# Kernel tuning notes

Hardware: AMD Instinct MI355X
Metric: run time of the kernel (lower is better)

## Reference

```python
import jax, jax.numpy as jnp
import numpy as np

B, N, I = 2, 2048, 768   # batch, note_seq_len, input_size
C, D = 256, 64           # num_classes, max_desc_len
LN_EPS = 1e-5


def setup_inputs() -> dict:
    key = jax.random.key(0)
    ks = jax.random.split(key, 10)
    x = jax.random.normal(ks[0], (B, N, I), dtype=jnp.float32)
    attention_masks = jnp.ones((B, N), dtype=jnp.int32)
    desc_emb = jax.random.normal(ks[1], (C, D, I), dtype=jnp.float32)
    # description mask: first token always valid, rest random 0/1
    dm_rest = jax.random.randint(ks[2], (C, D - 1), 0, 2, dtype=jnp.int32)
    desc_mask = jnp.concatenate([jnp.ones((C, 1), dtype=jnp.int32), dm_rest], axis=1)
    std = 0.03
    Wq = std * jax.random.normal(ks[3], (I, I), dtype=jnp.float32)
    Wk = std * jax.random.normal(ks[4], (I, I), dtype=jnp.float32)
    Wv = std * jax.random.normal(ks[5], (I, I), dtype=jnp.float32)
    Wo = std * jax.random.normal(ks[6], (1, I), dtype=jnp.float32)
    bo = jnp.zeros((1,), dtype=jnp.float32)
    ln_g = jnp.ones((I,), dtype=jnp.float32)
    ln_b = jnp.zeros((I,), dtype=jnp.float32)
    return {"x": x, "attention_masks": attention_masks, "desc_emb": desc_emb,
            "desc_mask": desc_mask, "Wq": Wq, "Wk": Wk, "Wv": Wv,
            "Wo": Wo, "bo": bo, "ln_g": ln_g, "ln_b": ln_b}


def reference(x, attention_masks, desc_emb, desc_mask, Wq, Wk, Wv, Wo, bo, ln_g, ln_b):
    scale = 1.0 / np.sqrt(np.float32(I))
    # projections (nn.Linear: y = x @ W.T)
    q = jnp.einsum('cdi,ji->cdj', desc_emb, Wq)        # [C, D, I]
    k = jnp.einsum('bni,ji->bnj', x, Wk)               # [B, N, I]
    v = jnp.einsum('bni,ji->bnj', x, Wv)               # [B, N, I]
    # cross-attention scores: [B, C, D, N]
    scores = jnp.einsum('cdi,bni->bcdn', q, k) * scale
    # double mask: desc token validity x note token validity
    mask = (desc_mask[None, :, :, None] * attention_masks[:, None, None, :]) > 0
    scores = jnp.where(mask, scores, jnp.float32(-1e9))
    attn = jax.nn.softmax(scores, axis=-1)             # over note tokens
    ctx = jnp.einsum('bcdn,bni->bcdi', attn, v)        # [B, C, D, I]
    dmask_f = (desc_mask > 0).astype(ctx.dtype)        # [C, D]
    ctx = ctx * dmask_f[None, :, :, None]
    denom = dmask_f.sum(axis=1)[None, :, None]          # [1, C, 1]
    pooled = ctx.sum(axis=2) / denom                    # [B, C, I]
    # layernorm over feature dim
    mu = pooled.mean(axis=-1, keepdims=True)
    var = jnp.mean((pooled - mu) ** 2, axis=-1, keepdims=True)
    y = (pooled - mu) * jax.lax.rsqrt(var + LN_EPS) * ln_g + ln_b
    out = jnp.einsum('bci,i->bc', y, Wo[0]) + bo[0]     # [B, C]
    return out
```

## Files before the change

### kernel.cpp

```cpp
#include <hip/hip_runtime.h>
#include <hip/hip_bf16.h>

#define BB 2
#define NN 2048
#define II 768
#define CC 256
#define DD 64
#define MM (CC * DD)

typedef __attribute__((ext_vector_type(8))) short short8;
typedef __attribute__((ext_vector_type(4))) float f32x4;

static constexpr float SCALE = 0.036084391824351615f;

__device__ __forceinline__ unsigned short f2bf(float f) {
  union { float f; unsigned int u; } v; v.f = f;
  unsigned int u = v.u;
  unsigned int r = u + 0x7fffu + ((u >> 16) & 1u);
  return (unsigned short)(r >> 16);
}
__device__ __forceinline__ float bf2f(unsigned short h) {
  union { unsigned int u; float f; } v; v.u = ((unsigned int)h) << 16;
  return v.f;
}

union U8 { unsigned short us[8]; uint4 v; };
struct US4 { unsigned short x, y, z, w; };

#define GLOAD_LDS16(gp, lp)                                                    \
  __builtin_amdgcn_global_load_lds(                                            \
      (const __attribute__((address_space(1))) unsigned int*)(gp),             \
      (__attribute__((address_space(3))) unsigned int*)(lp), 16, 0, 0)

__global__ __launch_bounds__(256)
void cvt_scan_kernel(const float* __restrict__ demb, const float* __restrict__ x,
                     const float* __restrict__ Wq, const float* __restrict__ Wk,
                     const float* __restrict__ Wv, const int* __restrict__ dmask,
                     unsigned short* __restrict__ Qb, unsigned short* __restrict__ xb,
                     unsigned short* __restrict__ Wqb, unsigned short* __restrict__ Wkb,
                     unsigned short* __restrict__ Wvb,
                     int* __restrict__ idx, int* __restrict__ cstart,
                     int* __restrict__ ccnt, int* __restrict__ meta)
{
  if (blockIdx.x == gridDim.x - 1) {
    const int c = threadIdx.x;
    int4 dmv[16];
    const int4* src = (const int4*)(dmask + c * 64);
    int cnt = 0;
    #pragma unroll
    for (int u = 0; u < 16; ++u) {
      dmv[u] = src[u];
      cnt += (dmv[u].x != 0) + (dmv[u].y != 0) + (dmv[u].z != 0) + (dmv[u].w != 0);
    }
    __shared__ int s[256];
    s[c] = cnt;
    __syncthreads();
    for (int off = 1; off < 256; off <<= 1) {
      int v = (c >= off) ? s[c - off] : 0;
      __syncthreads();
      s[c] += v;
      __syncthreads();
    }
    const int excl = s[c] - cnt;
    cstart[c] = excl;
    ccnt[c] = cnt;
    int j = excl;
    #pragma unroll
    for (int u = 0; u < 16; ++u) {
      if (dmv[u].x) idx[j++] = c * 64 + u * 4 + 0;
      if (dmv[u].y) idx[j++] = c * 64 + u * 4 + 1;
      if (dmv[u].z) idx[j++] = c * 64 + u * 4 + 2;
      if (dmv[u].w) idx[j++] = c * 64 + u * 4 + 3;
    }
    if (c == 255) {
      int mv = s[255];
      int mpad = (mv + 127) & ~127;
      for (int t = mv; t < mpad; ++t) idx[t] = 0;
      meta[0] = mpad;
    }
  }
  const int NF_DEMB = 3145728;
  const int NF_X    = 786432;
  const int NF_W    = 147456;
  const int NF_TOT  = NF_DEMB + NF_X + 3 * NF_W;
  for (int i = blockIdx.x * 256 + threadIdx.x; i < NF_TOT; i += gridDim.x * 256) {
    const float* src; unsigned short* dst; int off;
    if (i < NF_DEMB) {
      if (dmask[i / 192] == 0) continue;
      src = demb; dst = Qb; off = i;
    }
    else if (i < NF_DEMB + NF_X) { src = x; dst = xb; off = i - NF_DEMB; }
    else if (i < NF_DEMB + NF_X + NF_W) { src = Wq; dst = Wqb; off = i - NF_DEMB - NF_X; }
    else if (i < NF_DEMB + NF_X + 2 * NF_W) { src = Wk; dst = Wkb; off = i - NF_DEMB - NF_X - NF_W; }
    else { src = Wv; dst = Wvb; off = i - NF_DEMB - NF_X - 2 * NF_W; }
    float4 v = *(const float4*)(src + (size_t)off * 4);
    US4 o; o.x = f2bf(v.x); o.y = f2bf(v.y); o.z = f2bf(v.z); o.w = f2bf(v.w);
    *(US4*)(dst + (size_t)off * 4) = o;
  }
}

__global__ __launch_bounds__(256, 2)
void proj3(const unsigned short* __restrict__ Qb,
           const unsigned short* __restrict__ xb,
           const unsigned short* __restrict__ Wqb,
           const unsigned short* __restrict__ Wkb,
           const unsigned short* __restrict__ Wvb,
           unsigned short* __restrict__ Qp,
           unsigned short* __restrict__ Kp,
           unsigned short* __restrict__ Vt,
           const int* __restrict__ gidx, const int* __restrict__ meta)
{
  const int T = blockIdx.x;
  const int j0 = (T % 6) * 128;
  const int t = T / 6;
  const int mode = (t < 128) ? 0 : ((t < 160) ? 1 : 2);
  const int m0 = (mode == 0 ? t : (mode == 1 ? t - 128 : t - 160)) * 128;
  if (mode == 0 && m0 >= meta[0]) return;
  const unsigned short* A = (mode == 0) ? Qb : xb;
  const unsigned short* W = (mode == 0) ? Wqb : (mode == 1 ? Wkb : Wvb);

  const int tid = threadIdx.x;
  const int lane = tid & 63, wv = tid >> 6;
  const int lrow = lane & 15, khi = lane >> 4;
  const int wr = wv >> 1, wc = wv & 1;

  __shared__ __align__(16) unsigned short smem[128 * 128];
  unsigned short* a_lds = smem;
  unsigned short* b_lds = smem + 128 * 64;

  int rowsrc[4];
  #pragma unroll
  for (int u = 0; u < 4; ++u) {
    int row = m0 + ((u * 256 + tid) >> 3);
    rowsrc[u] = (mode == 0) ? gidx[row] : row;
  }

  f32x4 acc[4][4] = {};

  for (int kc = 0; kc < 12; ++kc) {
    const int k0 = kc * 64;
    __syncthreads();
    #pragma unroll
    for (int u = 0; u < 4; ++u) {
      int idx = u * 256 + tid;
      int row = idx >> 3, g = idx & 7;
      int sg = g ^ (row & 7);
      GLOAD_LDS16(A + (size_t)rowsrc[u] * II + k0 + sg * 8, &a_lds[idx * 8]);
      GLOAD_LDS16(W + (size_t)(j0 + row) * II + k0 + sg * 8, &b_lds[idx * 8]);
    }
    __syncthreads();
    #pragma unroll
    for (int s = 0; s < 2; ++s) {
      short8 af[4], bf[4];
      #pragma unroll
      for (int m = 0; m < 4; ++m) {
        int ar = wr * 64 + m * 16 + lrow;
        int g = s * 4 + khi;
        af[m] = *(const short8*)&a_lds[(ar * 8 + (g ^ (ar & 7))) * 8];
      }
      #pragma unroll
      for (int f = 0; f < 4; ++f) {
        int br = wc * 64 + f * 16 + lrow;
        int g = s * 4 + khi;
        bf[f] = *(const short8*)&b_lds[(br * 8 + (g ^ (br & 7))) * 8];
      }
      #pragma unroll
      for (int m = 0; m < 4; ++m)
        #pragma unroll
        for (int f = 0; f < 4; ++f)
          acc[m][f] = __builtin_amdgcn_mfma_f32_16x16x32_bf16(af[m], bf[f], acc[m][f], 0, 0, 0);
    }
  }

  if (mode != 2) {
    unsigned short* out = (mode == 0) ? Qp : Kp;
    __syncthreads();
    #pragma unroll
    for (int m = 0; m < 4; ++m)
      #pragma unroll
      for (int r = 0; r < 4; ++r) {
        const int row = wr * 64 + m * 16 + khi * 4 + r;
        const int s8 = (row & 7) << 3;
        #pragma unroll
        for (int f = 0; f < 4; ++f) {
          int col = wc * 64 + f * 16 + lrow;
          smem[row * 128 + (col ^ s8)] = f2bf(acc[m][f][r]);
        }
      }
    __syncthreads();
    #pragma unroll
    for (int u = 0; u < 8; ++u) {
      int idx = u * 256 + tid;
      int row = idx >> 4, q = idx & 15;
      int gcol = (q ^ (row & 7)) << 3;
      *(uint4*)(out + (size_t)(m0 + row) * II + j0 + gcol) =
          *(const uint4*)&smem[row * 128 + q * 8];
    }
  } else {
    #pragma unroll
    for (int m = 0; m < 4; ++m)
      #pragma unroll
      for (int f = 0; f < 4; ++f)
        #pragma unroll
        for (int r = 0; r < 4; ++r) {
          int row = m0 + wr * 64 + m * 16 + khi * 4 + r;
          int col = j0 + wc * 64 + f * 16 + lrow;
          int bb = row >> 11, n = row & (NN - 1);
          Vt[((size_t)bb * II + col) * NN + n] = f2bf(acc[m][f][r]);
        }
  }
}

__global__ __launch_bounds__(256, 4)
void attn_gemm1(const unsigned short* __restrict__ Qp,
                const unsigned short* __restrict__ Kp,
                const int* __restrict__ amask, const int* __restrict__ meta,
                float* __restrict__ lpart_out,
                unsigned short* __restrict__ P_out)
{
  const int m0 = blockIdx.z * 128;
  if (m0 >= meta[0]) return;
  const int ny = blockIdx.x;
  const int n0 = ny * 128;
  const int b  = blockIdx.y;
  const int tid = threadIdx.x;
  const int lane = tid & 63, wv = tid >> 6;
  const int lrow = lane & 15, khi = lane >> 4;
  const int wr = wv >> 1, wc = wv & 1;

  __shared__ __align__(16) unsigned short smem[128 * 128];
  unsigned short* a_lds = smem;
  unsigned short* b_lds = smem + 128 * 64;
  __shared__ float red_lds[128 * 2];

  const unsigned short* Kb = Kp + (size_t)b * NN * II;

  f32x4 acc[4][4] = {};

  for (int kc = 0; kc < 12; ++kc) {
    const int k0 = kc * 64;
    __syncthreads();
    #pragma unroll
    for (int u = 0; u < 4; ++u) {
      int idx = u * 256 + tid;
      int row = idx >> 3, g = idx & 7;
      int sg = g ^ (row & 7);
      GLOAD_LDS16(Qp + (size_t)(m0 + row) * II + k0 + sg * 8, &a_lds[idx * 8]);
      GLOAD_LDS16(Kb + (size_t)(n0 + row) * II + k0 + sg * 8, &b_lds[idx * 8]);
    }
    __syncthreads();
    #pragma unroll
    for (int s = 0; s < 2; ++s) {
      short8 af[4], bf[4];
      #pragma unroll
      for (int m = 0; m < 4; ++m) {
        int ar = wr * 64 + m * 16 + lrow;
        int g = s * 4 + khi;
        af[m] = *(const short8*)&a_lds[(ar * 8 + (g ^ (ar & 7))) * 8];
      }
      #pragma unroll
      for (int f = 0; f < 4; ++f) {
        int br = wc * 64 + f * 16 + lrow;
        int g = s * 4 + khi;
        bf[f] = *(const short8*)&b_lds[(br * 8 + (g ^ (br & 7))) * 8];
      }
      #pragma unroll
      for (int m = 0; m < 4; ++m)
        #pragma unroll
        for (int f = 0; f < 4; ++f)
          acc[m][f] = __builtin_amdgcn_mfma_f32_16x16x32_bf16(af[m], bf[f], acc[m][f], 0, 0, 0);
    }
  }

  float msk[4];
  #pragma unroll
  for (int f = 0; f < 4; ++f)
    msk[f] = (amask[b * NN + n0 + wc * 64 + f * 16 + lrow] != 0) ? 1.0f : 0.0f;

  __syncthreads();

  #pragma unroll
  for (int m = 0; m < 4; ++m) {
    #pragma unroll
    for (int r = 0; r < 4; ++r) {
      const int row = wr * 64 + m * 16 + khi * 4 + r;
      const int s8 = (row & 7) << 3;
      float rs = 0.0f;
      #pragma unroll
      for (int f = 0; f < 4; ++f) {
        float pe = msk[f] * __expf(acc[m][f][r] * SCALE);
        rs += pe;
        int col = wc * 64 + f * 16 + lrow;
        smem[row * 128 + (col ^ s8)] = f2bf(pe);
      }
      rs += __shfl_xor(rs, 1); rs += __shfl_xor(rs, 2);
      rs += __shfl_xor(rs, 4); rs += __shfl_xor(rs, 8);
      if (lrow == 0) red_lds[row * 2 + wc] = rs;
    }
  }
  __syncthreads();
  if (tid < 128)
    lpart_out[((size_t)(b * 16 + ny) << 14) + m0 + tid] =
        red_lds[tid * 2] + red_lds[tid * 2 + 1];
  unsigned short* Pb = P_out + (size_t)b * MM * NN;
  #pragma unroll
  for (int u = 0; u < 8; ++u) {
    int idx = u * 256 + tid;
    int row = idx >> 4, q = idx & 15;
    int gcol = (q ^ (row & 7)) << 3;
    *(uint4*)(Pb + (size_t)(m0 + row) * NN + n0 + gcol) =
        *(const uint4*)&smem[row * 128 + q * 8];
  }
}

__global__ __launch_bounds__(256)
void ppred_kernel(const unsigned short* __restrict__ P,
                  const float* __restrict__ lpart,
                  const int* __restrict__ cstart, const int* __restrict__ ccnt,
                  unsigned short* __restrict__ pp)
{
  const int c = blockIdx.x, b = blockIdx.y;
  const int tid = threadIdx.x;
  const int cs = cstart[c], cnt = ccnt[c];
  __shared__ float wgt[64];
  if (tid < cnt) {
    float lv = 0.0f;
    #pragma unroll
    for (int nt = 0; nt < 16; ++nt)
      lv += lpart[(((size_t)(b * 16 + nt)) << 14) + cs + tid];
    wgt[tid] = 1.0f / lv;
  }
  __syncthreads();
  const float invd = 1.0f / (float)cnt;
  float acc[8] = {};
  const unsigned short* Pr = P + ((size_t)b * MM + cs) * NN + tid * 8;
  #pragma unroll 4
  for (int d = 0; d < cnt; ++d) {
    U8 v; v.v = *(const uint4*)(Pr + (size_t)d * NN);
    float w = wgt[d];
    #pragma unroll
    for (int e = 0; e < 8; ++e) acc[e] += w * bf2f(v.us[e]);
  }
  U8 o;
  #pragma unroll
  for (int e = 0; e < 8; ++e) o.us[e] = f2bf(acc[e] * invd);
  *(uint4*)(pp + ((size_t)(b * CC + c)) * NN + tid * 8) = o.v;
}

__global__ __launch_bounds__(256, 2)
void pv_gemm(const unsigned short* __restrict__ pp,
             const unsigned short* __restrict__ Vt,
             float* __restrict__ pooled0, float* __restrict__ pooled1)
{
  const int m0 = blockIdx.x * 64;
  const int j0 = blockIdx.y * 64;
  const int b  = m0 >> 8;
  const int z  = blockIdx.z;
  const int tid = threadIdx.x;
  const int lane = tid & 63, wv = tid >> 6;
  const int lrow = lane & 15, khi = lane >> 4;

  __shared__ __align__(16) unsigned short a_lds[64 * 128];
  __shared__ __align__(16) unsigned short b_lds[64 * 128];

  f32x4 acc[4] = {};

  for (int kc = z * 8; kc < z * 8 + 8; ++kc) {
    const int k0 = kc * 128;
    __syncthreads();
    #pragma unroll
    for (int u = 0; u < 4; ++u) {
      int idx = u * 256 + tid;
      int row = idx >> 4, g = idx & 15;
      int sg = g ^ (row & 7);
      GLOAD_LDS16(pp + (size_t)(m0 + row) * NN + k0 + sg * 8, &a_lds[idx * 8]);
      GLOAD_LDS16(Vt + ((size_t)b * II + j0 + row) * NN + k0 + sg * 8, &b_lds[idx * 8]);
    }
    __syncthreads();
    #pragma unroll
    for (int s = 0; s < 4; ++s) {
      int g = s * 4 + khi;
      int ar = 16 * wv + lrow;
      short8 af = *(const short8*)&a_lds[(ar * 16 + (g ^ (ar & 7))) * 8];
      #pragma unroll
      for (int f = 0; f < 4; ++f) {
        int br = f * 16 + lrow;
        short8 bfr = *(const short8*)&b_lds[(br * 16 + (g ^ (br & 7))) * 8];
        acc[f] = __builtin_amdgcn_mfma_f32_16x16x32_bf16(af, bfr, acc[f], 0, 0, 0);
      }
    }
  }
  float* out = z ? pooled1 : pooled0;
  #pragma unroll
  for (int f = 0; f < 4; ++f)
    #pragma unroll
    for (int r = 0; r < 4; ++r) {
      int row = m0 + 16 * wv + khi * 4 + r;
      int col = j0 + f * 16 + lrow;
      out[(size_t)row * II + col] = acc[f][r];
    }
}

__global__ __launch_bounds__(256)
void ln_out_kernel(const float* __restrict__ pooled0, const float* __restrict__ pooled1,
                   const float* __restrict__ g, const float* __restrict__ beta,
                   const float* __restrict__ Wo, const float* __restrict__ bo,
                   float* __restrict__ out)
{
  const int bc = blockIdx.x;
  const int tid = threadIdx.x;
  const int lane = tid & 63, wv = tid >> 6;
  const float* r0 = pooled0 + (size_t)bc * II;
  const float* r1 = pooled1 + (size_t)bc * II;
  float x0 = r0[tid] + r1[tid];
  float x1 = r0[tid + 256] + r1[tid + 256];
  float x2 = r0[tid + 512] + r1[tid + 512];
  float s = x0 + x1 + x2;
  float sq = x0 * x0 + x1 * x1 + x2 * x2;
  #pragma unroll
  for (int m = 1; m < 64; m <<= 1) { s += __shfl_xor(s, m); sq += __shfl_xor(sq, m); }
  __shared__ float red[8];
  if (lane == 0) { red[wv] = s; red[4 + wv] = sq; }
  __syncthreads();
  s = red[0] + red[1] + red[2] + red[3];
  sq = red[4] + red[5] + red[6] + red[7];
  const float mu = s * (1.0f / 768.0f);
  const float var = sq * (1.0f / 768.0f) - mu * mu;
  const float rs = rsqrtf(var + 1e-5f);
  float dot = ((x0 - mu) * rs * g[tid] + beta[tid]) * Wo[tid]
            + ((x1 - mu) * rs * g[tid + 256] + beta[tid + 256]) * Wo[tid + 256]
            + ((x2 - mu) * rs * g[tid + 512] + beta[tid + 512]) * Wo[tid + 512];
  #pragma unroll
  for (int m = 1; m < 64; m <<= 1) dot += __shfl_xor(dot, m);
  __syncthreads();
  if (lane == 0) red[wv] = dot;
  __syncthreads();
  if (tid == 0) out[bc] = red[0] + red[1] + red[2] + red[3] + bo[0];
}

extern "C" void kernel_launch(void* const* d_in, const int* in_sizes, int n_in,
                              void* d_out, int out_size, void* d_ws, size_t ws_size,
                              hipStream_t stream) {
  const float* x     = (const float*)d_in[0];
  const int*   amask = (const int*)d_in[1];
  const float* demb  = (const float*)d_in[2];
  const int*   dmask = (const int*)d_in[3];
  const float* Wq    = (const float*)d_in[4];
  const float* Wk    = (const float*)d_in[5];
  const float* Wv    = (const float*)d_in[6];
  const float* Wo    = (const float*)d_in[7];
  const float* bo    = (const float*)d_in[8];
  const float* lng   = (const float*)d_in[9];
  const float* lnb   = (const float*)d_in[10];

  char* ws = (char*)d_ws;
  const size_t OFF_QB  = 0;
  const size_t OFF_XB  = OFF_QB + (size_t)MM * II * 2;
  const size_t OFF_WQB = OFF_XB + (size_t)BB * NN * II * 2;
  const size_t OFF_WKB = OFF_WQB + (size_t)II * II * 2;
  const size_t OFF_WVB = OFF_WKB + (size_t)II * II * 2;
  const size_t OFF_P   = 0;
  const size_t OFF_PL0 = 0;
  const size_t OFF_PL1 = (size_t)BB * CC * II * 4;
  const size_t OFF_QP = (size_t)BB * MM * NN * 2;
  const size_t OFF_KP = OFF_QP + (size_t)MM * II * 2;
  const size_t OFF_VT = OFF_KP + (size_t)BB * NN * II * 2;
  const size_t OFF_LP = OFF_VT + (size_t)BB * II * NN * 2;
  const size_t OFF_PP = OFF_LP + (size_t)BB * 16 * MM * 4;
  const size_t OFF_IDX = OFF_PP + (size_t)BB * CC * NN * 2;
  const size_t OFF_CS  = OFF_IDX + (size_t)MM * 4;
  const size_t OFF_CNT = OFF_CS + (size_t)CC * 4;
  const size_t OFF_MET = OFF_CNT + (size_t)CC * 4;

  unsigned short* Qb  = (unsigned short*)(ws + OFF_QB);
  unsigned short* xb  = (unsigned short*)(ws + OFF_XB);
  unsigned short* Wqb = (unsigned short*)(ws + OFF_WQB);
  unsigned short* Wkb = (unsigned short*)(ws + OFF_WKB);
  unsigned short* Wvb = (unsigned short*)(ws + OFF_WVB);
  unsigned short* P   = (unsigned short*)(ws + OFF_P);
  float* pooled0 = (float*)(ws + OFF_PL0);
  float* pooled1 = (float*)(ws + OFF_PL1);
  unsigned short* Qp  = (unsigned short*)(ws + OFF_QP);
  unsigned short* Kp  = (unsigned short*)(ws + OFF_KP);
  unsigned short* Vt  = (unsigned short*)(ws + OFF_VT);
  float* l_part = (float*)(ws + OFF_LP);
  unsigned short* pp = (unsigned short*)(ws + OFF_PP);
  int* idx    = (int*)(ws + OFF_IDX);
  int* cstart = (int*)(ws + OFF_CS);
  int* ccnt   = (int*)(ws + OFF_CNT);
  int* meta   = (int*)(ws + OFF_MET);

  cvt_scan_kernel<<<2048, 256, 0, stream>>>(demb, x, Wq, Wk, Wv, dmask,
                                            Qb, xb, Wqb, Wkb, Wvb,
                                            idx, cstart, ccnt, meta);

  proj3<<<192 * 6, 256, 0, stream>>>(Qb, xb, Wqb, Wkb, Wvb, Qp, Kp, Vt, idx, meta);

  attn_gemm1<<<dim3(NN / 128, BB, MM / 128), 256, 0, stream>>>(
      Qp, Kp, amask, meta, l_part, P);
  ppred_kernel<<<dim3(CC, BB), 256, 0, stream>>>(P, l_part, cstart, ccnt, pp);

  pv_gemm<<<dim3((BB * CC) / 64, II / 64, 2), 256, 0, stream>>>(pp, Vt, pooled0, pooled1);
  ln_out_kernel<<<BB * CC, 256, 0, stream>>>(pooled0, pooled1, lng, lnb, Wo, bo, (float*)d_out);
}
```

Before: 156.7 us.

## Increase split parallelism in ppred and pv_gemm, drop LDS row-sum reduction in attn_gemm1

attn_gemm1 now writes per-wave-column row sums straight to global memory instead of reducing them through shared memory. That removes red_lds and lets launch_bounds ask for 5 blocks per CU. ppred_kernel is split across two N halves with 128 threads each and sums 32 partials instead of 16. pv_gemm uses a 4-way split-K in place of 2-way, and ln_out sums four partial buffers. The aim is more concurrent blocks in the smaller kernels and higher occupancy in the attention GEMM, at the cost of extra partial-buffer traffic and possible register pressure.

```diff
diff --git a/kernel.cpp b/kernel.cpp
--- a/kernel.cpp
+++ b/kernel.cpp
@@ -211,7 +211,7 @@
   }
 }
 
-__global__ __launch_bounds__(256, 4)
+__global__ __launch_bounds__(256, 5)
 void attn_gemm1(const unsigned short* __restrict__ Qp,
                 const unsigned short* __restrict__ Kp,
                 const int* __restrict__ amask, const int* __restrict__ meta,
@@ -231,7 +231,6 @@
   __shared__ __align__(16) unsigned short smem[128 * 128];
   unsigned short* a_lds = smem;
   unsigned short* b_lds = smem + 128 * 64;
-  __shared__ float red_lds[128 * 2];
 
   const unsigned short* Kb = Kp + (size_t)b * NN * II;
 
@@ -279,6 +278,7 @@
 
   __syncthreads();
 
+  float* lrow_out = lpart_out + (((size_t)(b * 32 + ny * 2 + wc)) << 14) + m0;
   #pragma unroll
   for (int m = 0; m < 4; ++m) {
     #pragma unroll
@@ -295,13 +295,10 @@
       }
       rs += __shfl_xor(rs, 1); rs += __shfl_xor(rs, 2);
       rs += __shfl_xor(rs, 4); rs += __shfl_xor(rs, 8);
-      if (lrow == 0) red_lds[row * 2 + wc] = rs;
+      if (lrow == 0) lrow_out[row] = rs;
     }
   }
   __syncthreads();
-  if (tid < 128)
-    lpart_out[((size_t)(b * 16 + ny) << 14) + m0 + tid] =
-        red_lds[tid * 2] + red_lds[tid * 2 + 1];
   unsigned short* Pb = P_out + (size_t)b * MM * NN;
   #pragma unroll
   for (int u = 0; u < 8; ++u) {
@@ -313,27 +310,28 @@
   }
 }
 
-__global__ __launch_bounds__(256)
+__global__ __launch_bounds__(128)
 void ppred_kernel(const unsigned short* __restrict__ P,
                   const float* __restrict__ lpart,
                   const int* __restrict__ cstart, const int* __restrict__ ccnt,
                   unsigned short* __restrict__ pp)
 {
   const int c = blockIdx.x, b = blockIdx.y;
+  const int nz = blockIdx.z * 1024;
   const int tid = threadIdx.x;
   const int cs = cstart[c], cnt = ccnt[c];
   __shared__ float wgt[64];
   if (tid < cnt) {
     float lv = 0.0f;
     #pragma unroll
-    for (int nt = 0; nt < 16; ++nt)
-      lv += lpart[(((size_t)(b * 16 + nt)) << 14) + cs + tid];
+    for (int nt = 0; nt < 32; ++nt)
+      lv += lpart[(((size_t)(b * 32 + nt)) << 14) + cs + tid];
     wgt[tid] = 1.0f / lv;
   }
   __syncthreads();
   const float invd = 1.0f / (float)cnt;
   float acc[8] = {};
-  const unsigned short* Pr = P + ((size_t)b * MM + cs) * NN + tid * 8;
+  const unsigned short* Pr = P + ((size_t)b * MM + cs) * NN + nz + tid * 8;
   #pragma unroll 4
   for (int d = 0; d < cnt; ++d) {
     U8 v; v.v = *(const uint4*)(Pr + (size_t)d * NN);
@@ -344,13 +342,13 @@
   U8 o;
   #pragma unroll
   for (int e = 0; e < 8; ++e) o.us[e] = f2bf(acc[e] * invd);
-  *(uint4*)(pp + ((size_t)(b * CC + c)) * NN + tid * 8) = o.v;
+  *(uint4*)(pp + ((size_t)(b * CC + c)) * NN + nz + tid * 8) = o.v;
 }
 
 __global__ __launch_bounds__(256, 2)
 void pv_gemm(const unsigned short* __restrict__ pp,
              const unsigned short* __restrict__ Vt,
-             float* __restrict__ pooled0, float* __restrict__ pooled1)
+             float* __restrict__ pooled)
 {
   const int m0 = blockIdx.x * 64;
   const int j0 = blockIdx.y * 64;
@@ -365,7 +363,7 @@
 
   f32x4 acc[4] = {};
 
-  for (int kc = z * 8; kc < z * 8 + 8; ++kc) {
+  for (int kc = z * 4; kc < z * 4 + 4; ++kc) {
     const int k0 = kc * 128;
     __syncthreads();
     #pragma unroll
@@ -390,7 +388,7 @@
       }
     }
   }
-  float* out = z ? pooled1 : pooled0;
+  float* out = pooled + (size_t)z * (BB * CC * II);
   #pragma unroll
   for (int f = 0; f < 4; ++f)
     #pragma unroll
@@ -402,7 +400,7 @@
 }
 
 __global__ __launch_bounds__(256)
-void ln_out_kernel(const float* __restrict__ pooled0, const float* __restrict__ pooled1,
+void ln_out_kernel(const float* __restrict__ pooled,
                    const float* __restrict__ g, const float* __restrict__ beta,
                    const float* __restrict__ Wo, const float* __restrict__ bo,
                    float* __restrict__ out)
@@ -410,11 +408,11 @@
   const int bc = blockIdx.x;
   const int tid = threadIdx.x;
   const int lane = tid & 63, wv = tid >> 6;
-  const float* r0 = pooled0 + (size_t)bc * II;
-  const float* r1 = pooled1 + (size_t)bc * II;
-  float x0 = r0[tid] + r1[tid];
-  float x1 = r0[tid + 256] + r1[tid + 256];
-  float x2 = r0[tid + 512] + r1[tid + 512];
+  const size_t PSZ = (size_t)BB * CC * II;
+  const float* r0 = pooled + (size_t)bc * II;
+  float x0 = r0[tid]       + r0[PSZ + tid]       + r0[2 * PSZ + tid]       + r0[3 * PSZ + tid];
+  float x1 = r0[tid + 256] + r0[PSZ + tid + 256] + r0[2 * PSZ + tid + 256] + r0[3 * PSZ + tid + 256];
+  float x2 = r0[tid + 512] + r0[PSZ + tid + 512] + r0[2 * PSZ + tid + 512] + r0[3 * PSZ + tid + 512];
   float s = x0 + x1 + x2;
   float sq = x0 * x0 + x1 * x1 + x2 * x2;
   #pragma unroll
@@ -460,13 +458,12 @@
   const size_t OFF_WKB = OFF_WQB + (size_t)II * II * 2;
   const size_t OFF_WVB = OFF_WKB + (size_t)II * II * 2;
   const size_t OFF_P   = 0;
-  const size_t OFF_PL0 = 0;
-  const size_t OFF_PL1 = (size_t)BB * CC * II * 4;
+  const size_t OFF_PL  = 0;
   const size_t OFF_QP = (size_t)BB * MM * NN * 2;
   const size_t OFF_KP = OFF_QP + (size_t)MM * II * 2;
   const size_t OFF_VT = OFF_KP + (size_t)BB * NN * II * 2;
   const size_t OFF_LP = OFF_VT + (size_t)BB * II * NN * 2;
-  const size_t OFF_PP = OFF_LP + (size_t)BB * 16 * MM * 4;
+  const size_t OFF_PP = OFF_LP + (size_t)BB * 32 * MM * 4;
   const size_t OFF_IDX = OFF_PP + (size_t)BB * CC * NN * 2;
   const size_t OFF_CS  = OFF_IDX + (size_t)MM * 4;
   const size_t OFF_CNT = OFF_CS + (size_t)CC * 4;
@@ -478,12 +475,13 @@
   unsigned short* Wkb = (unsigned short*)(ws + OFF_WKB);
   unsigned short* Wvb = (unsigned short*)(ws + OFF_WVB);
   unsigned short* P   = (unsigned short*)(ws + OFF_P);
-  float* pooled0 = (float*)(ws + OFF_PL0);
-  float* pooled1 = (float*)(ws + OFF_PL1);
+  float* pooled = (float*)(ws + OFF_PL);
   unsigned short* Qp  = (unsigned short*)(ws + OFF_QP);
   unsigned short* Kp  = (unsigned short*)(ws + OFF_KP);
   unsigned short* Vt  = (unsigned short*)(ws + OFF_VT);
   float* l_part = (float*)(ws + OFF_LP);
+  (void)l_part;
+  float* lpart = (float*)(ws + OFF_LP);
   unsigned short* pp = (unsigned short*)(ws + OFF_PP);
   int* idx    = (int*)(ws + OFF_IDX);
   int* cstart = (int*)(ws + OFF_CS);
@@ -497,9 +495,9 @@
   proj3<<<192 * 6, 256, 0, stream>>>(Qb, xb, Wqb, Wkb, Wvb, Qp, Kp, Vt, idx, meta);
 
   attn_gemm1<<<dim3(NN / 128, BB, MM / 128), 256, 0, stream>>>(
-      Qp, Kp, amask, meta, l_part, P);
-  ppred_kernel<<<dim3(CC, BB), 256, 0, stream>>>(P, l_part, cstart, ccnt, pp);
-
-  pv_gemm<<<dim3((BB * CC) / 64, II / 64, 2), 256, 0, stream>>>(pp, Vt, pooled0, pooled1);
-  ln_out_kernel<<<BB * CC, 256, 0, stream>>>(pooled0, pooled1, lng, lnb, Wo, bo, (float*)d_out);
-}
+      Qp, Kp, amask, meta, lpart, P);
+  ppred_kernel<<<dim3(CC, BB, 2), 128, 0, stream>>>(P, lpart, cstart, ccnt, pp);
+
+  pv_gemm<<<dim3((BB * CC) / 64, II / 64, 4), 256, 0, stream>>>(pp, Vt, pooled);
+  ln_out_kernel<<<BB * CC, 256, 0, stream>>>(pooled, lng, lnb, Wo, bo, (float*)d_out);
+}
```

Result: slower. 213.0 us (+35.9%).
